# Kernel optimization log

Hardware: AMD Instinct MI355X
Metric: run time of the kernel (lower is better)

## Reference

```python
import jax, jax.numpy as jnp
import numpy as np

NUM_NODES = 200000
MAX_DEG = 32
BATCH = 8192
MEM_DIM = 128
TIME_DIM = 64
TAU = 0.1
W_S, L_S = 10, 3
W_L, L_L = 5, 10
W_T, L_T = 5, 8
NEG = -1e30


def setup_inputs() -> dict:
    key = jax.random.key(0)
    ks = jax.random.split(key, 8)
    return {
        "source_nodes": jax.random.randint(ks[0], (BATCH,), 0, NUM_NODES),
        # source times in [0.5, 1.0) so most neighbors (times in [0,1)) are temporally valid
        "current_times": jax.random.uniform(ks[1], (BATCH,), jnp.float32, 0.5, 1.0),
        "neighbor_ids": jax.random.randint(ks[2], (NUM_NODES, MAX_DEG), 0, NUM_NODES),
        "neighbor_times": jax.random.uniform(ks[3], (NUM_NODES, MAX_DEG)),
        "memory_states": jax.random.normal(ks[4], (NUM_NODES, MEM_DIM)),
        "restart_w": jax.random.normal(ks[5], (MEM_DIM + TIME_DIM,)) * 0.05,
        "restart_b": jnp.zeros(()),
        "time_w": jax.random.normal(ks[6], (TIME_DIM,)),
        "time_b": jax.random.normal(ks[7], (TIME_DIM,)),
    }


def _pack(first, rest, B, W, L):
    # first: [B*W], rest: [L-1, B*W] -> [B, W, L]
    x = jnp.concatenate([first[None], rest], 0)  # [L, B*W]
    return x.T.reshape(B, W, L)


def _plain_walks(key, src, t0, nb_ids, nb_ts, num_walks, length):
    """Temporal-biased walks (Eq. 7): P(u,t'|v,t) = softmax(t'/tau) over neighbors with t' < t."""
    B = src.shape[0]
    n0 = jnp.repeat(src, num_walks)                      # [B*W]
    t0r = jnp.repeat(t0, num_walks)

    def step(carry, k):
        cur_n, cur_t, alive = carry
        ni = nb_ids[cur_n]                               # [BW, D] gather
        nt = nb_ts[cur_n]
        valid = nt < cur_t[:, None]
        has = jnp.any(valid, axis=-1)
        logits = jnp.where(valid, nt / TAU, NEG)         # softmax shift by t_max handled by categorical
        idx = jax.random.categorical(k, logits)          # [BW]
        nn = jnp.take_along_axis(ni, idx[:, None], 1)[:, 0]
        ntm = jnp.take_along_axis(nt, idx[:, None], 1)[:, 0]
        alive = alive & has
        cur_n = jnp.where(alive, nn, cur_n)
        cur_t = jnp.where(alive, ntm, cur_t)
        outs = (jnp.where(alive, nn, 0),
                jnp.where(alive, ntm, 0.0),
                alive.astype(jnp.float32))
        return (cur_n, cur_t, alive), outs

    keys = jax.random.split(key, length - 1)
    init = (n0, t0r, jnp.ones(n0.shape, bool))
    _, (ns, ts, ms) = jax.lax.scan(step, init, keys)
    nodes = _pack(n0, ns, B, num_walks, length)
    times = _pack(t0r, ts, B, num_walks, length)
    masks = _pack(jnp.ones_like(t0r), ms, B, num_walks, length)
    return nodes, times, masks


def _tawr_walks(key, src, t0, nb_ids, nb_ts, memory_states,
                restart_w, restart_b, time_w, time_b, num_walks, length):
    """Temporal anonymous walks with learnable restart rho = sigmoid(w^T [m_u || Phi(t)] + b)."""
    B = src.shape[0]
    n0 = jnp.repeat(src, num_walks)
    t0r = jnp.repeat(t0, num_walks)

    def step(carry, k):
        cur_n, cur_t, alive = carry
        k1, k2 = jax.random.split(k)
        # restart probability from memory state + time encoding Phi(t) = cos(t*w + b)
        phi = jnp.cos(cur_t[:, None] * time_w[None, :] + time_b[None, :])   # [BW, T]
        mem = memory_states[cur_n]                                           # [BW, M]
        feat = jnp.concatenate([mem, phi], axis=-1)
        rho = jax.nn.sigmoid(feat @ restart_w + restart_b)                   # [BW]
        restart = jax.random.uniform(k1, rho.shape) < rho
        # temporal-biased neighbor sampling
        ni = nb_ids[cur_n]
        nt = nb_ts[cur_n]
        valid = nt < cur_t[:, None]
        has = jnp.any(valid, axis=-1)
        logits = jnp.where(valid, nt / TAU, NEG)
        idx = jax.random.categorical(k2, logits)
        nn = jnp.take_along_axis(ni, idx[:, None], 1)[:, 0]
        ntm = jnp.take_along_axis(nt, idx[:, None], 1)[:, 0]
        # restart overrides neighbor step and keeps the walk alive
        nn = jnp.where(restart, n0, nn)
        ntm = jnp.where(restart, t0r, ntm)
        alive = alive & (restart | has)
        cur_n = jnp.where(alive, nn, cur_n)
        cur_t = jnp.where(alive, ntm, cur_t)
        m = alive.astype(jnp.float32)
        outs = (jnp.where(alive, nn, 0),
                jnp.where(alive, ntm, 0.0),
                m,
                (restart & alive).astype(jnp.float32),
                rho * m)
        return (cur_n, cur_t, alive), outs

    keys = jax.random.split(key, length - 1)
    init = (n0, t0r, jnp.ones(n0.shape, bool))
    _, (ns, ts, ms, rs, rhos) = jax.lax.scan(step, init, keys)
    z = jnp.zeros_like(t0r)
    nodes = _pack(n0, ns, B, num_walks, length)
    times = _pack(t0r, ts, B, num_walks, length)
    masks = _pack(jnp.ones_like(t0r), ms, B, num_walks, length)
    rflag = _pack(z, rs, B, num_walks, length)
    rho_o = _pack(z, rhos, B, num_walks, length)
    return nodes, times, masks, rflag, rho_o


def reference(source_nodes, current_times, neighbor_ids, neighbor_times,
              memory_states, restart_w, restart_b, time_w, time_b):
    key = jax.random.key(42)
    k1, k2, k3 = jax.random.split(key, 3)
    short = _plain_walks(k1, source_nodes, current_times, neighbor_ids, neighbor_times, W_S, L_S)
    longw = _plain_walks(k2, source_nodes, current_times, neighbor_ids, neighbor_times, W_L, L_L)
    tawr = _tawr_walks(k3, source_nodes, current_times, neighbor_ids, neighbor_times,
                       memory_states, restart_w, restart_b, time_w, time_b, W_T, L_T)
    return short + longw + tawr
```

## Files before the change

kernel.cpp:

```cpp
#include <hip/hip_runtime.h>
#include <stdint.h>
#include <math.h>


namespace {

constexpr int kB   = 8192;
constexpr int kWS  = 10, kLS = 3;
constexpr int kWL  = 5,  kLL = 10;
constexpr int kWT  = 5,  kLT = 8;
constexpr int kBWS = kB * kWS;
constexpr int kBWL = kB * kWL;
constexpr int kBWT = kB * kWT;
constexpr int kTotal = kBWS + kBWL + kBWT;

constexpr int O_SN = 0;
constexpr int O_ST = O_SN + kBWS * kLS;
constexpr int O_SM = O_ST + kBWS * kLS;
constexpr int O_LN = O_SM + kBWS * kLS;
constexpr int O_LT = O_LN + kBWL * kLL;
constexpr int O_LM = O_LT + kBWL * kLL;
constexpr int O_TN = O_LM + kBWL * kLL;
constexpr int O_TT = O_TN + kBWT * kLT;
constexpr int O_TM = O_TT + kBWT * kLT;
constexpr int O_TR = O_TM + kBWT * kLT;
constexpr int O_TQ = O_TR + kBWT * kLT;

struct Keys {
  uint32_t sk[kLS - 1][2];
  uint32_t lk[kLL - 1][2];
  uint32_t tu[kLT - 1][2];
  uint32_t tc[kLT - 1][2];
};

}

__host__ __device__ static inline void tf2x32(uint32_t k0, uint32_t k1,
                                              uint32_t x0, uint32_t x1,
                                              uint32_t& o0, uint32_t& o1) {
  uint32_t ks2 = k0 ^ k1 ^ 0x1BD11BDAu;
#define TFR(r) { x0 += x1; x1 = (x1 << (r)) | (x1 >> (32 - (r))); x1 ^= x0; }
  x0 += k0; x1 += k1;
  TFR(13) TFR(15) TFR(26) TFR(6)
  x0 += k1;  x1 += ks2 + 1u;
  TFR(17) TFR(29) TFR(16) TFR(24)
  x0 += ks2; x1 += k0 + 2u;
  TFR(13) TFR(15) TFR(26) TFR(6)
  x0 += k0;  x1 += k1 + 3u;
  TFR(17) TFR(29) TFR(16) TFR(24)
  x0 += k1;  x1 += ks2 + 4u;
  TFR(13) TFR(15) TFR(26) TFR(6)
  x0 += ks2; x1 += k0 + 5u;
#undef TFR
  o0 = x0; o1 = x1;
}

__device__ __forceinline__ uint32_t rbits32(uint32_t k0, uint32_t k1, uint32_t j) {
  uint32_t a, b;
  tf2x32(k0, k1, 0u, j, a, b);
  return a ^ b;
}

__device__ __forceinline__ float bits_to_u01(uint32_t bits) {
  return __uint_as_float((bits >> 9) | 0x3f800000u) - 1.0f;
}

__device__ __forceinline__ float gumbel_of(uint32_t k0, uint32_t k1, uint32_t j) {
  float u = bits_to_u01(rbits32(k0, k1, j));
  if (u == 0.0f) u = 1.17549435e-38f;
  return -logf(-logf(u));
}

struct CatRes { int idx; float bt; bool has; };

__device__ __forceinline__ CatRes categorical32(uint32_t k0, uint32_t k1,
                                                uint32_t j0,
                                                const float* __restrict__ row_t,
                                                float t) {
  CatRes r; r.idx = 0; r.bt = 0.0f; r.has = false;
  float best = -INFINITY;
  const float4* row4 = (const float4*)row_t;
#pragma unroll 2
  for (int q = 0; q < 8; ++q) {
    float4 v4 = row4[q];
    float nv0 = v4.x, nv1 = v4.y, nv2 = v4.z, nv3 = v4.w;
#define CAT_ONE(E, NV)                                                       \
    {                                                                        \
      int d = q * 4 + (E);                                                   \
      float ntd = (NV);                                                      \
      bool valid = ntd < t;                                                  \
      r.has |= valid;                                                        \
      float g = gumbel_of(k0, k1, j0 + (uint32_t)d);                         \
      float logit = valid ? __fdiv_rn(ntd, 0.1f) : -1e30f;                   \
      float v = __fadd_rn(g, logit);                                         \
      if (v > best) { best = v; r.idx = d; r.bt = ntd; }                     \
    }
    CAT_ONE(0, nv0) CAT_ONE(1, nv1) CAT_ONE(2, nv2) CAT_ONE(3, nv3)
#undef CAT_ONE
  }
  return r;
}

template <int W, int L>
__device__ void plain_walk(int bw, const uint32_t keys[][2],
                           const int* __restrict__ src, const float* __restrict__ ct,
                           const int* __restrict__ nbi, const float* __restrict__ nbt,
                           float* __restrict__ on, float* __restrict__ ot,
                           float* __restrict__ om) {
  int b = bw / W;
  int cur = src[b];
  float t = ct[b];
  int obase = bw * L;
  on[obase] = (float)cur; ot[obase] = t; om[obase] = 1.0f;
  bool alive = true;
  for (int s = 0; s < L - 1; ++s) {
    float wn = 0.0f, wt = 0.0f, wm = 0.0f;
    if (alive) {
      uint32_t j0 = (uint32_t)bw * 32u;
      CatRes c = categorical32(keys[s][0], keys[s][1], j0,
                               nbt + (size_t)cur * 32, t);
      if (c.has) {
        cur = nbi[(size_t)cur * 32 + c.idx];
        t = c.bt;
        wn = (float)cur; wt = t; wm = 1.0f;
      } else {
        alive = false;
      }
    }
    int o = obase + s + 1;
    on[o] = wn; ot[o] = wt; om[o] = wm;
  }
}

__device__ void tawr_walk(int bw, const Keys& K,
                          const int* __restrict__ src, const float* __restrict__ ct,
                          const int* __restrict__ nbi, const float* __restrict__ nbt,
                          const float* __restrict__ mem, const float* __restrict__ rw,
                          const float* __restrict__ rb, const float* __restrict__ tw,
                          const float* __restrict__ tb,
                          float* __restrict__ on, float* __restrict__ ot,
                          float* __restrict__ om, float* __restrict__ orf,
                          float* __restrict__ orh) {
  int b = bw / kWT;
  int n0 = src[b];
  float t0 = ct[b];
  float rbv = rb[0];
  int cur = n0;
  float t = t0;
  int obase = bw * kLT;
  on[obase] = (float)n0; ot[obase] = t0; om[obase] = 1.0f;
  orf[obase] = 0.0f; orh[obase] = 0.0f;
  bool alive = true;

  for (int s = 0; s < kLT - 1; ++s) {
    float wn = 0.0f, wt = 0.0f, wm = 0.0f, wr = 0.0f, wq = 0.0f;
    if (alive) {
      float acc = 0.0f;
      const float4* mrow = (const float4*)(mem + (size_t)cur * 128);
      const float4* rw4 = (const float4*)rw;
#pragma unroll 4
      for (int q = 0; q < 32; ++q) {
        float4 a = mrow[q];
        float4 w = rw4[q];
        acc = __fadd_rn(acc, __fmul_rn(a.x, w.x));
        acc = __fadd_rn(acc, __fmul_rn(a.y, w.y));
        acc = __fadd_rn(acc, __fmul_rn(a.z, w.z));
        acc = __fadd_rn(acc, __fmul_rn(a.w, w.w));
      }
#pragma unroll 4
      for (int j = 0; j < 64; ++j) {
        float phi = cosf(__fadd_rn(__fmul_rn(t, tw[j]), tb[j]));
        acc = __fadd_rn(acc, __fmul_rn(phi, rw[128 + j]));
      }
      float z = __fadd_rn(acc, rbv);
      float rho = __fdiv_rn(1.0f, __fadd_rn(1.0f, expf(-z)));

      float u = bits_to_u01(rbits32(K.tu[s][0], K.tu[s][1], (uint32_t)bw));
      bool restart = u < rho;

      bool has = false;
      int nn = 0;
      float ntm = 0.0f;
      if (!restart) {
        uint32_t j0 = (uint32_t)bw * 32u;
        CatRes c = categorical32(K.tc[s][0], K.tc[s][1], j0,
                                 nbt + (size_t)cur * 32, t);
        has = c.has;
        if (has) {
          nn = nbi[(size_t)cur * 32 + c.idx];
          ntm = c.bt;
        }
      } else {
        nn = n0;
        ntm = t0;
      }

      if (restart || has) {
        cur = nn; t = ntm;
        wn = (float)nn; wt = ntm; wm = 1.0f;
        wr = restart ? 1.0f : 0.0f;
        wq = rho;
      } else {
        alive = false;
      }
    }
    int o = obase + s + 1;
    on[o] = wn; ot[o] = wt; om[o] = wm; orf[o] = wr; orh[o] = wq;
  }
}

__global__ __launch_bounds__(256) void walks_kernel(
    const int* __restrict__ src, const float* __restrict__ ct,
    const int* __restrict__ nbi, const float* __restrict__ nbt,
    const float* __restrict__ mem, const float* __restrict__ rw,
    const float* __restrict__ rb, const float* __restrict__ tw,
    const float* __restrict__ tb, float* __restrict__ out, Keys K) {
  int tid = blockIdx.x * blockDim.x + threadIdx.x;
  if (tid >= kTotal) return;
  if (tid < kBWS) {
    plain_walk<kWS, kLS>(tid, K.sk, src, ct, nbi, nbt,
                         out + O_SN, out + O_ST, out + O_SM);
  } else if (tid < kBWS + kBWL) {
    plain_walk<kWL, kLL>(tid - kBWS, K.lk, src, ct, nbi, nbt,
                         out + O_LN, out + O_LT, out + O_LM);
  } else {
    tawr_walk(tid - kBWS - kBWL, K, src, ct, nbi, nbt, mem, rw, rb, tw, tb,
              out + O_TN, out + O_TT, out + O_TM, out + O_TR, out + O_TQ);
  }
}

extern "C" void kernel_launch(void* const* d_in, const int* in_sizes, int n_in,
                              void* d_out, int out_size, void* d_ws, size_t ws_size,
                              hipStream_t stream) {
  (void)in_sizes; (void)n_in; (void)out_size; (void)d_ws; (void)ws_size;

  const int*   src = (const int*)d_in[0];
  const float* ct  = (const float*)d_in[1];
  const int*   nbi = (const int*)d_in[2];
  const float* nbt = (const float*)d_in[3];
  const float* mem = (const float*)d_in[4];
  const float* rw  = (const float*)d_in[5];
  const float* rb  = (const float*)d_in[6];
  const float* tw  = (const float*)d_in[7];
  const float* tb  = (const float*)d_in[8];
  float* out = (float*)d_out;

  Keys K;
  uint32_t k1[2], k2[2], k3[2];
  tf2x32(0u, 42u, 0u, 0u, k1[0], k1[1]);
  tf2x32(0u, 42u, 0u, 1u, k2[0], k2[1]);
  tf2x32(0u, 42u, 0u, 2u, k3[0], k3[1]);
  for (uint32_t s = 0; s < kLS - 1; ++s)
    tf2x32(k1[0], k1[1], 0u, s, K.sk[s][0], K.sk[s][1]);
  for (uint32_t s = 0; s < kLL - 1; ++s)
    tf2x32(k2[0], k2[1], 0u, s, K.lk[s][0], K.lk[s][1]);
  for (uint32_t s = 0; s < kLT - 1; ++s) {
    uint32_t ks[2];
    tf2x32(k3[0], k3[1], 0u, s, ks[0], ks[1]);
    tf2x32(ks[0], ks[1], 0u, 0u, K.tu[s][0], K.tu[s][1]);
    tf2x32(ks[0], ks[1], 0u, 1u, K.tc[s][0], K.tc[s][1]);
  }

  dim3 grid((kTotal + 255) / 256);
  walks_kernel<<<grid, dim3(256), 0, stream>>>(src, ct, nbi, nbt, mem, rw, rb,
                                               tw, tb, out, K);
}
```

Baseline: 374.3 us.

## Split walks into two kernels with four lanes per walk

Each walk is now handled by a group of four lanes instead of one thread. The 32-neighbor categorical sampling is split eight entries per lane and combined with a shuffle argmax. The TAWR restart dot product computes partial products per lane in shared memory, and every lane sums them serially in the original order, so the float rounding matches the reference. Output writes are spread across the lanes, and the plain and TAWR walks run as separate kernels so their different costs no longer diverge inside a warp. The aim is to cut per-thread serial latency and raise memory-level parallelism, at the cost of redundant summation and more launches.

```diff
diff --git a/kernel.cpp b/kernel.cpp
--- a/kernel.cpp
+++ b/kernel.cpp
@@ -12,7 +12,6 @@
 constexpr int kBWS = kB * kWS;
 constexpr int kBWL = kB * kWL;
 constexpr int kBWT = kB * kWT;
-constexpr int kTotal = kBWS + kBWL + kBWT;
 
 constexpr int O_SN = 0;
 constexpr int O_ST = O_SN + kBWS * kLS;
@@ -32,6 +31,8 @@
   uint32_t tu[kLT - 1][2];
   uint32_t tc[kLT - 1][2];
 };
+
+constexpr int kSlotStride = 68;
 
 }
 
@@ -71,54 +72,58 @@
   return -logf(-logf(u));
 }
 
-struct CatRes { int idx; float bt; bool has; };
-
-__device__ __forceinline__ CatRes categorical32(uint32_t k0, uint32_t k1,
-                                                uint32_t j0,
-                                                const float* __restrict__ row_t,
-                                                float t) {
-  CatRes r; r.idx = 0; r.bt = 0.0f; r.has = false;
+struct Cat4 { int idx; float bt; bool has; };
+
+__device__ __forceinline__ Cat4 categorical_g4(uint32_t k0, uint32_t k1,
+                                               uint32_t j0,
+                                               const float* __restrict__ row_t,
+                                               float t, int r) {
+  const float4* row4 = (const float4*)row_t;
+  float4 v0 = row4[2 * r];
+  float4 v1 = row4[2 * r + 1];
+  float nv[8] = {v0.x, v0.y, v0.z, v0.w, v1.x, v1.y, v1.z, v1.w};
   float best = -INFINITY;
-  const float4* row4 = (const float4*)row_t;
-#pragma unroll 2
-  for (int q = 0; q < 8; ++q) {
-    float4 v4 = row4[q];
-    float nv0 = v4.x, nv1 = v4.y, nv2 = v4.z, nv3 = v4.w;
-#define CAT_ONE(E, NV)                                                       \
-    {                                                                        \
-      int d = q * 4 + (E);                                                   \
-      float ntd = (NV);                                                      \
-      bool valid = ntd < t;                                                  \
-      r.has |= valid;                                                        \
-      float g = gumbel_of(k0, k1, j0 + (uint32_t)d);                         \
-      float logit = valid ? __fdiv_rn(ntd, 0.1f) : -1e30f;                   \
-      float v = __fadd_rn(g, logit);                                         \
-      if (v > best) { best = v; r.idx = d; r.bt = ntd; }                     \
-    }
-    CAT_ONE(0, nv0) CAT_ONE(1, nv1) CAT_ONE(2, nv2) CAT_ONE(3, nv3)
-#undef CAT_ONE
-  }
-  return r;
+  int bidx = 0;
+  float bbt = 0.0f;
+#pragma unroll
+  for (int e = 0; e < 8; ++e) {
+    int d = 8 * r + e;
+    float ntd = nv[e];
+    bool valid = ntd < t;
+    float g = gumbel_of(k0, k1, j0 + (uint32_t)d);
+    float logit = valid ? __fdiv_rn(ntd, 0.1f) : -1e30f;
+    float v = __fadd_rn(g, logit);
+    if (v > best) { best = v; bidx = d; bbt = ntd; }
+  }
+#pragma unroll
+  for (int m = 1; m <= 2; m <<= 1) {
+    float ov = __shfl_xor(best, m);
+    int   oi = __shfl_xor(bidx, m);
+    float ob = __shfl_xor(bbt, m);
+    if (ov > best || (ov == best && oi < bidx)) { best = ov; bidx = oi; bbt = ob; }
+  }
+  Cat4 c; c.idx = bidx; c.bt = bbt; c.has = best > -1e29f;
+  return c;
 }
 
 template <int W, int L>
-__device__ void plain_walk(int bw, const uint32_t keys[][2],
-                           const int* __restrict__ src, const float* __restrict__ ct,
-                           const int* __restrict__ nbi, const float* __restrict__ nbt,
-                           float* __restrict__ on, float* __restrict__ ot,
-                           float* __restrict__ om) {
+__device__ void plain_walk_g4(int bw, int r, const uint32_t keys[][2],
+                              const int* __restrict__ src, const float* __restrict__ ct,
+                              const int* __restrict__ nbi, const float* __restrict__ nbt,
+                              float* __restrict__ on, float* __restrict__ ot,
+                              float* __restrict__ om) {
   int b = bw / W;
   int cur = src[b];
   float t = ct[b];
   int obase = bw * L;
-  on[obase] = (float)cur; ot[obase] = t; om[obase] = 1.0f;
+  if (r == 0) { on[obase] = (float)cur; ot[obase] = t; }
+  else if (r == 1) { om[obase] = 1.0f; }
   bool alive = true;
   for (int s = 0; s < L - 1; ++s) {
     float wn = 0.0f, wt = 0.0f, wm = 0.0f;
     if (alive) {
-      uint32_t j0 = (uint32_t)bw * 32u;
-      CatRes c = categorical32(keys[s][0], keys[s][1], j0,
-                               nbt + (size_t)cur * 32, t);
+      Cat4 c = categorical_g4(keys[s][0], keys[s][1], (uint32_t)bw * 32u,
+                              nbt + (size_t)cur * 32, t, r);
       if (c.has) {
         cur = nbi[(size_t)cur * 32 + c.idx];
         t = c.bt;
@@ -128,19 +133,37 @@
       }
     }
     int o = obase + s + 1;
-    on[o] = wn; ot[o] = wt; om[o] = wm;
-  }
-}
-
-__device__ void tawr_walk(int bw, const Keys& K,
-                          const int* __restrict__ src, const float* __restrict__ ct,
-                          const int* __restrict__ nbi, const float* __restrict__ nbt,
-                          const float* __restrict__ mem, const float* __restrict__ rw,
-                          const float* __restrict__ rb, const float* __restrict__ tw,
-                          const float* __restrict__ tb,
-                          float* __restrict__ on, float* __restrict__ ot,
-                          float* __restrict__ om, float* __restrict__ orf,
-                          float* __restrict__ orh) {
+    if (r == 0) on[o] = wn;
+    else if (r == 1) ot[o] = wt;
+    else if (r == 2) om[o] = wm;
+  }
+}
+
+__global__ __launch_bounds__(256) void plain_kernel(
+    const int* __restrict__ src, const float* __restrict__ ct,
+    const int* __restrict__ nbi, const float* __restrict__ nbt,
+    float* __restrict__ out, Keys K) {
+  int tid = blockIdx.x * blockDim.x + threadIdx.x;
+  int gid = tid >> 2;
+  int r = tid & 3;
+  if (gid < kBWL) {
+    plain_walk_g4<kWL, kLL>(gid, r, K.lk, src, ct, nbi, nbt,
+                            out + O_LN, out + O_LT, out + O_LM);
+  } else {
+    plain_walk_g4<kWS, kLS>(gid - kBWL, r, K.sk, src, ct, nbi, nbt,
+                            out + O_SN, out + O_ST, out + O_SM);
+  }
+}
+
+__device__ void tawr_g4(int bw, int r, float* __restrict__ slot, const Keys& K,
+                        const int* __restrict__ src, const float* __restrict__ ct,
+                        const int* __restrict__ nbi, const float* __restrict__ nbt,
+                        const float* __restrict__ mem, const float* __restrict__ rw,
+                        const float* __restrict__ rb, const float* __restrict__ tw,
+                        const float* __restrict__ tb,
+                        float* __restrict__ on, float* __restrict__ ot,
+                        float* __restrict__ om, float* __restrict__ orf,
+                        float* __restrict__ orh) {
   int b = bw / kWT;
   int n0 = src[b];
   float t0 = ct[b];
@@ -148,33 +171,65 @@
   int cur = n0;
   float t = t0;
   int obase = bw * kLT;
-  on[obase] = (float)n0; ot[obase] = t0; om[obase] = 1.0f;
-  orf[obase] = 0.0f; orh[obase] = 0.0f;
+  if (r == 0) { on[obase] = (float)n0; ot[obase] = t0; }
+  else if (r == 1) { om[obase] = 1.0f; orf[obase] = 0.0f; }
+  else if (r == 2) { orh[obase] = 0.0f; }
   bool alive = true;
+
+  const float4* rw4 = (const float4*)rw;
+  const float4* tw4 = (const float4*)tw;
+  const float4* tb4 = (const float4*)tb;
 
   for (int s = 0; s < kLT - 1; ++s) {
     float wn = 0.0f, wt = 0.0f, wm = 0.0f, wr = 0.0f, wq = 0.0f;
     if (alive) {
+      const float4* mrow = (const float4*)(mem + (size_t)cur * 128);
       float acc = 0.0f;
-      const float4* mrow = (const float4*)(mem + (size_t)cur * 128);
-      const float4* rw4 = (const float4*)rw;
-#pragma unroll 4
-      for (int q = 0; q < 32; ++q) {
-        float4 a = mrow[q];
-        float4 w = rw4[q];
-        acc = __fadd_rn(acc, __fmul_rn(a.x, w.x));
-        acc = __fadd_rn(acc, __fmul_rn(a.y, w.y));
-        acc = __fadd_rn(acc, __fmul_rn(a.z, w.z));
-        acc = __fadd_rn(acc, __fmul_rn(a.w, w.w));
-      }
-#pragma unroll 4
-      for (int j = 0; j < 64; ++j) {
-        float phi = cosf(__fadd_rn(__fmul_rn(t, tw[j]), tb[j]));
-        acc = __fadd_rn(acc, __fmul_rn(phi, rw[128 + j]));
-      }
+#pragma unroll
+      for (int ph = 0; ph < 2; ++ph) {
+#pragma unroll
+        for (int q = 0; q < 4; ++q) {
+          int f4 = 16 * ph + 4 * r + q;
+          float4 a = mrow[f4];
+          float4 w = rw4[f4];
+          float4 p;
+          p.x = __fmul_rn(a.x, w.x); p.y = __fmul_rn(a.y, w.y);
+          p.z = __fmul_rn(a.z, w.z); p.w = __fmul_rn(a.w, w.w);
+          *(float4*)(slot + 16 * r + 4 * q) = p;
+        }
+        asm volatile("" ::: "memory");
+#pragma unroll
+        for (int q = 0; q < 16; ++q) {
+          float4 p = *(const float4*)(slot + 4 * q);
+          acc = __fadd_rn(acc, p.x); acc = __fadd_rn(acc, p.y);
+          acc = __fadd_rn(acc, p.z); acc = __fadd_rn(acc, p.w);
+        }
+        asm volatile("" ::: "memory");
+      }
+#pragma unroll
+      for (int q = 0; q < 4; ++q) {
+        int f4 = 4 * r + q;
+        float4 w = tw4[f4];
+        float4 bb = tb4[f4];
+        float4 rwp = rw4[32 + f4];
+        float4 p;
+        p.x = __fmul_rn(cosf(__fadd_rn(__fmul_rn(t, w.x), bb.x)), rwp.x);
+        p.y = __fmul_rn(cosf(__fadd_rn(__fmul_rn(t, w.y), bb.y)), rwp.y);
+        p.z = __fmul_rn(cosf(__fadd_rn(__fmul_rn(t, w.z), bb.z)), rwp.z);
+        p.w = __fmul_rn(cosf(__fadd_rn(__fmul_rn(t, w.w), bb.w)), rwp.w);
+        *(float4*)(slot + 16 * r + 4 * q) = p;
+      }
+      asm volatile("" ::: "memory");
+#pragma unroll
+      for (int q = 0; q < 16; ++q) {
+        float4 p = *(const float4*)(slot + 4 * q);
+        acc = __fadd_rn(acc, p.x); acc = __fadd_rn(acc, p.y);
+        acc = __fadd_rn(acc, p.z); acc = __fadd_rn(acc, p.w);
+      }
+      asm volatile("" ::: "memory");
+
       float z = __fadd_rn(acc, rbv);
       float rho = __fdiv_rn(1.0f, __fadd_rn(1.0f, expf(-z)));
-
       float u = bits_to_u01(rbits32(K.tu[s][0], K.tu[s][1], (uint32_t)bw));
       bool restart = u < rho;
 
@@ -182,9 +237,8 @@
       int nn = 0;
       float ntm = 0.0f;
       if (!restart) {
-        uint32_t j0 = (uint32_t)bw * 32u;
-        CatRes c = categorical32(K.tc[s][0], K.tc[s][1], j0,
-                                 nbt + (size_t)cur * 32, t);
+        Cat4 c = categorical_g4(K.tc[s][0], K.tc[s][1], (uint32_t)bw * 32u,
+                                nbt + (size_t)cur * 32, t, r);
         has = c.has;
         if (has) {
           nn = nbi[(size_t)cur * 32 + c.idx];
@@ -205,28 +259,25 @@
       }
     }
     int o = obase + s + 1;
-    on[o] = wn; ot[o] = wt; om[o] = wm; orf[o] = wr; orh[o] = wq;
-  }
-}
-
-__global__ __launch_bounds__(256) void walks_kernel(
+    if (r == 0) { on[o] = wn; ot[o] = wt; }
+    else if (r == 1) { om[o] = wm; orf[o] = wr; }
+    else if (r == 2) { orh[o] = wq; }
+  }
+}
+
+__global__ __launch_bounds__(256) void tawr_kernel(
     const int* __restrict__ src, const float* __restrict__ ct,
     const int* __restrict__ nbi, const float* __restrict__ nbt,
     const float* __restrict__ mem, const float* __restrict__ rw,
     const float* __restrict__ rb, const float* __restrict__ tw,
     const float* __restrict__ tb, float* __restrict__ out, Keys K) {
+  __shared__ float plds[64 * kSlotStride];
   int tid = blockIdx.x * blockDim.x + threadIdx.x;
-  if (tid >= kTotal) return;
-  if (tid < kBWS) {
-    plain_walk<kWS, kLS>(tid, K.sk, src, ct, nbi, nbt,
-                         out + O_SN, out + O_ST, out + O_SM);
-  } else if (tid < kBWS + kBWL) {
-    plain_walk<kWL, kLL>(tid - kBWS, K.lk, src, ct, nbi, nbt,
-                         out + O_LN, out + O_LT, out + O_LM);
-  } else {
-    tawr_walk(tid - kBWS - kBWL, K, src, ct, nbi, nbt, mem, rw, rb, tw, tb,
-              out + O_TN, out + O_TT, out + O_TM, out + O_TR, out + O_TQ);
-  }
+  int gid = tid >> 2;
+  int r = tid & 3;
+  int ws = threadIdx.x >> 2;
+  tawr_g4(gid, r, plds + ws * kSlotStride, K, src, ct, nbi, nbt, mem, rw, rb,
+          tw, tb, out + O_TN, out + O_TT, out + O_TM, out + O_TR, out + O_TQ);
 }
 
 extern "C" void kernel_launch(void* const* d_in, const int* in_sizes, int n_in,
@@ -261,7 +312,7 @@
     tf2x32(ks[0], ks[1], 0u, 1u, K.tc[s][0], K.tc[s][1]);
   }
 
-  dim3 grid((kTotal + 255) / 256);
-  walks_kernel<<<grid, dim3(256), 0, stream>>>(src, ct, nbi, nbt, mem, rw, rb,
-                                               tw, tb, out, K);
-}
+  tawr_kernel<<<dim3(640), dim3(256), 0, stream>>>(src, ct, nbi, nbt, mem, rw,
+                                                   rb, tw, tb, out, K);
+  plain_kernel<<<dim3(1920), dim3(256), 0, stream>>>(src, ct, nbi, nbt, out, K);
+}
```

Result: faster. 328.9 us (-12.1%).
